# Kernel optimization log

Hardware: AMD Instinct MI355X
Metric: run time of the kernel (lower is better)

## Reference

```python
import jax, jax.numpy as jnp
import numpy as np
from jax.scipy.special import logsumexp

SPARSITY = 0.0


def setup_inputs() -> dict:
    key = jax.random.key(0)
    k1, k2, k3, k4, k5 = jax.random.split(key, 5)
    N, M = 65536, 1024
    sample = jax.random.uniform(k1, (N, 2), dtype=jnp.float32)
    mu = jax.random.uniform(k2, (M, 2), dtype=jnp.float32)
    sigma_log = jax.random.uniform(k3, (M, 2), dtype=jnp.float32)
    theta = jax.random.normal(k4, (M,), dtype=jnp.float32)
    w = jax.random.normal(k5, (M, 1), dtype=jnp.float32)
    return {"sample": sample, "mu": mu, "sigma_log": sigma_log, "theta": theta, "w": w}


def reference(sample, mu, sigma_log, theta, w):
    # Anisotropic covariance entries: gamma_j = R(theta)^T diag(sig2) R(theta)
    sig2 = jnp.exp(-2.0 * sigma_log)            # [M,2], inverse variances
    a, b = sig2[:, 0], sig2[:, 1]
    c, s = jnp.cos(theta), jnp.sin(theta)
    g11 = a * c**2 + b * s**2                   # [M]
    g12 = (a - b) * c * s                       # [M]
    g22 = a * s**2 + b * c**2                   # [M]

    # Log weights: log_softmax(w) - sum(sigma_log) (normalization factor)
    wlog = jax.nn.log_softmax(w, axis=0)[:, 0] - sigma_log.sum(axis=1)  # [M]

    # All-pairs anisotropic quadratic form, fused per-coordinate (no [N,M,2] tensor)
    dx = sample[:, None, 0] - mu[None, :, 0]    # [N,M]
    dy = sample[:, None, 1] - mu[None, :, 1]    # [N,M]
    qf = g11 * dx * dx + 2.0 * g12 * dx * dy + g22 * dy * dy  # [N,M]

    # Log-density at each sample: logsumexp over mixture components
    ll = logsumexp(wlog[None, :] - qf, axis=1)  # [N]

    # Negative log-likelihood + sparsity penalty
    nll = -ll.sum() + SPARSITY * jnp.sqrt(jax.nn.softmax(w, axis=0)).sum()
    return nll
```

## Files before the change

kernel.cpp:

```cpp
#include <hip/hip_runtime.h>
#include <math.h>

#define LOG2E 1.4426950408889634f
#define LN2   0.6931471805599453f

typedef short bf8 __attribute__((ext_vector_type(8)));
typedef float f4  __attribute__((ext_vector_type(4)));

__device__ __forceinline__ unsigned short bf_hi(float x) {
    unsigned u = __float_as_uint(x);
    return (unsigned short)((u + 0x7FFFu + ((u >> 16) & 1u)) >> 16);
}

__global__ __launch_bounds__(1024) void gm_prep(
    const float* __restrict__ mu,
    const float* __restrict__ sigma_log,
    const float* __restrict__ theta,
    const float* __restrict__ w,
    unsigned* __restrict__ grec,
    float* __restrict__ out)
{
    const int j = threadIdx.x;
    const int lane = j & 63;
    const int wid  = j >> 6;

    const float wj = w[j];
    float e = __expf(wj);
    #pragma unroll
    for (int off = 32; off > 0; off >>= 1)
        e += __shfl_down(e, off, 64);
    __shared__ float ws[16];
    if (lane == 0) ws[wid] = e;
    __syncthreads();
    float tot = 0.0f;
    #pragma unroll
    for (int k = 0; k < 16; ++k) tot += ws[k];
    const float lse = __logf(tot);

    const float sl0 = sigma_log[2 * j + 0];
    const float sl1 = sigma_log[2 * j + 1];
    const float a = __expf(-2.0f * sl0);
    const float b = __expf(-2.0f * sl1);
    const float th = theta[j];
    const float c = __cosf(th);
    const float s = __sinf(th);

    const float g11 = a * c * c + b * s * s;
    const float g12 = (a - b) * c * s;
    const float g22 = a * s * s + b * c * c;
    const float mx = mu[2 * j + 0];
    const float my = mu[2 * j + 1];
    const float wlog = wj - lse - (sl0 + sl1);

    float cf[6];
    cf[0] = -g11 * LOG2E;
    cf[1] = -2.0f * g12 * LOG2E;
    cf[2] = -g22 * LOG2E;
    cf[3] = 2.0f * (g11 * mx + g12 * my) * LOG2E;
    cf[4] = 2.0f * (g12 * mx + g22 * my) * LOG2E;
    const float F = g11 * mx * mx + 2.0f * g12 * mx * my + g22 * my * my;
    cf[5] = (wlog - F) * LOG2E;

    unsigned short r[32];
    #pragma unroll
    for (int q = 0; q < 6; ++q) {
        const unsigned short h = bf_hi(cf[q]);
        const float hf = __uint_as_float((unsigned)h << 16);
        const unsigned short l = bf_hi(cf[q] - hf);
        r[q] = h; r[6 + q] = l; r[12 + q] = h;
    }
    #pragma unroll
    for (int q = 18; q < 32; ++q) r[q] = 0;
    unsigned* dst = grec + j * 20;
    #pragma unroll
    for (int k = 0; k < 16; ++k)
        dst[k] = ((unsigned)r[2 * k + 1] << 16) | r[2 * k];

    if (j == 0) out[0] = 0.0f;
}

__global__ __launch_bounds__(1024) void gm_main(
    const float* __restrict__ sample,
    const float4* __restrict__ grec4,
    float* __restrict__ out)
{
    __shared__ __align__(16) unsigned short wrec[1024 * 40];
    __shared__ __align__(16) unsigned short srec[256 * 40];
    __shared__ float psum[16 * 256];
    __shared__ float bsum[4];

    const int tid  = threadIdx.x;
    const int lane = tid & 63;
    const int wid  = tid >> 6;
    const int quad = lane >> 4;
    const int col  = lane & 15;

    float4* wl = (float4*)wrec;
    #pragma unroll
    for (int i = 0; i < 5; ++i)
        wl[i * 1024 + tid] = grec4[i * 1024 + tid];

    if (tid < 256) {
        const float2 sv = ((const float2*)sample)[blockIdx.x * 256 + tid];
        float f[6];
        f[0] = sv.x * sv.x; f[1] = sv.x * sv.y; f[2] = sv.y * sv.y;
        f[3] = sv.x; f[4] = sv.y; f[5] = 1.0f;
        unsigned short r[32];
        #pragma unroll
        for (int q = 0; q < 6; ++q) {
            const unsigned short h = bf_hi(f[q]);
            const float hf = __uint_as_float((unsigned)h << 16);
            const unsigned short l = bf_hi(f[q] - hf);
            r[q] = h; r[6 + q] = h; r[12 + q] = l;
        }
        #pragma unroll
        for (int q = 18; q < 32; ++q) r[q] = 0;
        unsigned* dst = (unsigned*)&srec[tid * 40];
        #pragma unroll
        for (int k = 0; k < 16; ++k)
            dst[k] = ((unsigned)r[2 * k + 1] << 16) | r[2 * k];
    }
    __syncthreads();

    bf8 afrag[4];
    #pragma unroll
    for (int ct = 0; ct < 4; ++ct)
        afrag[ct] = *(const bf8*)&wrec[(wid * 64 + ct * 16 + col) * 40 + quad * 8];

    const f4 zero = {0.0f, 0.0f, 0.0f, 0.0f};
    for (int st = 0; st < 16; ++st) {
        const bf8 bfrag = *(const bf8*)&srec[(st * 16 + col) * 40 + quad * 8];
        float acc = 0.0f;
        #pragma unroll
        for (int ct = 0; ct < 4; ++ct) {
            const f4 d = __builtin_amdgcn_mfma_f32_16x16x32_bf16(
                afrag[ct], bfrag, zero, 0, 0, 0);
            acc += (__builtin_amdgcn_exp2f(d[0]) + __builtin_amdgcn_exp2f(d[1]))
                 + (__builtin_amdgcn_exp2f(d[2]) + __builtin_amdgcn_exp2f(d[3]));
        }
        acc += __shfl_xor(acc, 16, 64);
        acc += __shfl_xor(acc, 32, 64);
        if (quad == 0) psum[wid * 256 + st * 16 + col] = acc;
    }
    __syncthreads();

    if (tid < 256) {
        float t = 0.0f;
        #pragma unroll
        for (int k = 0; k < 16; ++k) t += psum[k * 256 + tid];
        float v = -LN2 * __builtin_amdgcn_logf(t);
        #pragma unroll
        for (int off = 32; off > 0; off >>= 1)
            v += __shfl_down(v, off, 64);
        if ((tid & 63) == 0) bsum[tid >> 6] = v;
    }
    __syncthreads();
    if (tid == 0)
        atomicAdd(out, (bsum[0] + bsum[1]) + (bsum[2] + bsum[3]));
}

extern "C" void kernel_launch(void* const* d_in, const int* in_sizes, int n_in,
                              void* d_out, int out_size, void* d_ws, size_t ws_size,
                              hipStream_t stream) {
    const float* sample    = (const float*)d_in[0];
    const float* mu        = (const float*)d_in[1];
    const float* sigma_log = (const float*)d_in[2];
    const float* theta     = (const float*)d_in[3];
    const float* w         = (const float*)d_in[4];
    float* out = (float*)d_out;
    unsigned* grec = (unsigned*)d_ws;

    const int N = in_sizes[0] / 2;

    gm_prep<<<1, 1024, 0, stream>>>(mu, sigma_log, theta, w, grec, out);

    const int grid = N / 256;
    gm_main<<<grid, 1024, 0, stream>>>(sample, (const float4*)grec, out);
}
```

Baseline: 77.36 us.

## Fuse prep into main kernel and reduce via cooperative grid sync

Each block now recomputes the per-component coefficient records directly into shared memory instead of loading them from a separate single-block prep kernel. This removes one kernel launch and the serial dependency on it. The global atomic accumulation is replaced by per-block partials, a cooperative grid sync, and a final reduction in block 0. The cost is redundant transcendental work in all 256 blocks and a grid-wide barrier, and the grid must fit co-resident for the cooperative launch to succeed.

Result: slower. 160.4 us (+107.4%).

```diff
diff --git a/kernel.cpp b/kernel.cpp
--- a/kernel.cpp
+++ b/kernel.cpp
@@ -1,4 +1,5 @@
 #include <hip/hip_runtime.h>
+#include <hip/hip_cooperative_groups.h>
 #include <math.h>
 
 #define LOG2E 1.4426950408889634f
@@ -12,80 +13,18 @@
     return (unsigned short)((u + 0x7FFFu + ((u >> 16) & 1u)) >> 16);
 }
 
-__global__ __launch_bounds__(1024) void gm_prep(
+__global__ __launch_bounds__(1024) void gm_coop(
+    const float* __restrict__ sample,
     const float* __restrict__ mu,
     const float* __restrict__ sigma_log,
     const float* __restrict__ theta,
     const float* __restrict__ w,
-    unsigned* __restrict__ grec,
-    float* __restrict__ out)
-{
-    const int j = threadIdx.x;
-    const int lane = j & 63;
-    const int wid  = j >> 6;
-
-    const float wj = w[j];
-    float e = __expf(wj);
-    #pragma unroll
-    for (int off = 32; off > 0; off >>= 1)
-        e += __shfl_down(e, off, 64);
-    __shared__ float ws[16];
-    if (lane == 0) ws[wid] = e;
-    __syncthreads();
-    float tot = 0.0f;
-    #pragma unroll
-    for (int k = 0; k < 16; ++k) tot += ws[k];
-    const float lse = __logf(tot);
-
-    const float sl0 = sigma_log[2 * j + 0];
-    const float sl1 = sigma_log[2 * j + 1];
-    const float a = __expf(-2.0f * sl0);
-    const float b = __expf(-2.0f * sl1);
-    const float th = theta[j];
-    const float c = __cosf(th);
-    const float s = __sinf(th);
-
-    const float g11 = a * c * c + b * s * s;
-    const float g12 = (a - b) * c * s;
-    const float g22 = a * s * s + b * c * c;
-    const float mx = mu[2 * j + 0];
-    const float my = mu[2 * j + 1];
-    const float wlog = wj - lse - (sl0 + sl1);
-
-    float cf[6];
-    cf[0] = -g11 * LOG2E;
-    cf[1] = -2.0f * g12 * LOG2E;
-    cf[2] = -g22 * LOG2E;
-    cf[3] = 2.0f * (g11 * mx + g12 * my) * LOG2E;
-    cf[4] = 2.0f * (g12 * mx + g22 * my) * LOG2E;
-    const float F = g11 * mx * mx + 2.0f * g12 * mx * my + g22 * my * my;
-    cf[5] = (wlog - F) * LOG2E;
-
-    unsigned short r[32];
-    #pragma unroll
-    for (int q = 0; q < 6; ++q) {
-        const unsigned short h = bf_hi(cf[q]);
-        const float hf = __uint_as_float((unsigned)h << 16);
-        const unsigned short l = bf_hi(cf[q] - hf);
-        r[q] = h; r[6 + q] = l; r[12 + q] = h;
-    }
-    #pragma unroll
-    for (int q = 18; q < 32; ++q) r[q] = 0;
-    unsigned* dst = grec + j * 20;
-    #pragma unroll
-    for (int k = 0; k < 16; ++k)
-        dst[k] = ((unsigned)r[2 * k + 1] << 16) | r[2 * k];
-
-    if (j == 0) out[0] = 0.0f;
-}
-
-__global__ __launch_bounds__(1024) void gm_main(
-    const float* __restrict__ sample,
-    const float4* __restrict__ grec4,
+    float* __restrict__ part,
     float* __restrict__ out)
 {
     __shared__ __align__(16) unsigned short wrec[1024 * 40];
     __shared__ __align__(16) unsigned short srec[256 * 40];
+    __shared__ float ws[16];
     __shared__ float psum[16 * 256];
     __shared__ float bsum[4];
 
@@ -95,10 +34,58 @@
     const int quad = lane >> 4;
     const int col  = lane & 15;
 
-    float4* wl = (float4*)wrec;
+    const float wj = w[tid];
+    float e = __expf(wj);
     #pragma unroll
-    for (int i = 0; i < 5; ++i)
-        wl[i * 1024 + tid] = grec4[i * 1024 + tid];
+    for (int off = 32; off > 0; off >>= 1)
+        e += __shfl_down(e, off, 64);
+    if (lane == 0) ws[wid] = e;
+    __syncthreads();
+    float tot = 0.0f;
+    #pragma unroll
+    for (int k = 0; k < 16; ++k) tot += ws[k];
+    const float lse = __logf(tot);
+
+    {
+        const float sl0 = sigma_log[2 * tid + 0];
+        const float sl1 = sigma_log[2 * tid + 1];
+        const float a = __expf(-2.0f * sl0);
+        const float b = __expf(-2.0f * sl1);
+        const float th = theta[tid];
+        const float c = __cosf(th);
+        const float s = __sinf(th);
+
+        const float g11 = a * c * c + b * s * s;
+        const float g12 = (a - b) * c * s;
+        const float g22 = a * s * s + b * c * c;
+        const float mx = mu[2 * tid + 0];
+        const float my = mu[2 * tid + 1];
+        const float wlog = wj - lse - (sl0 + sl1);
+
+        float cf[6];
+        cf[0] = -g11 * LOG2E;
+        cf[1] = -2.0f * g12 * LOG2E;
+        cf[2] = -g22 * LOG2E;
+        cf[3] = 2.0f * (g11 * mx + g12 * my) * LOG2E;
+        cf[4] = 2.0f * (g12 * mx + g22 * my) * LOG2E;
+        const float F = g11 * mx * mx + 2.0f * g12 * mx * my + g22 * my * my;
+        cf[5] = (wlog - F) * LOG2E;
+
+        unsigned short r[32];
+        #pragma unroll
+        for (int q = 0; q < 6; ++q) {
+            const unsigned short h = bf_hi(cf[q]);
+            const float hf = __uint_as_float((unsigned)h << 16);
+            const unsigned short l = bf_hi(cf[q] - hf);
+            r[q] = h; r[6 + q] = l; r[12 + q] = h;
+        }
+        #pragma unroll
+        for (int q = 18; q < 32; ++q) r[q] = 0;
+        unsigned* dst = (unsigned*)&wrec[tid * 40];
+        #pragma unroll
+        for (int k = 0; k < 16; ++k)
+            dst[k] = ((unsigned)r[2 * k + 1] << 16) | r[2 * k];
+    }
 
     if (tid < 256) {
         const float2 sv = ((const float2*)sample)[blockIdx.x * 256 + tid];
@@ -156,7 +143,22 @@
     }
     __syncthreads();
     if (tid == 0)
-        atomicAdd(out, (bsum[0] + bsum[1]) + (bsum[2] + bsum[3]));
+        part[blockIdx.x] = (bsum[0] + bsum[1]) + (bsum[2] + bsum[3]);
+
+    __threadfence();
+    cooperative_groups::this_grid().sync();
+
+    if (blockIdx.x == 0 && tid < 256) {
+        float v = part[tid];
+        #pragma unroll
+        for (int off = 32; off > 0; off >>= 1)
+            v += __shfl_down(v, off, 64);
+        __shared__ float fs[4];
+        if ((tid & 63) == 0) fs[tid >> 6] = v;
+        __syncthreads();
+        if (tid == 0)
+            out[0] = (fs[0] + fs[1]) + (fs[2] + fs[3]);
+    }
 }
 
 extern "C" void kernel_launch(void* const* d_in, const int* in_sizes, int n_in,
@@ -167,13 +169,14 @@
     const float* sigma_log = (const float*)d_in[2];
     const float* theta     = (const float*)d_in[3];
     const float* w         = (const float*)d_in[4];
-    float* out = (float*)d_out;
-    unsigned* grec = (unsigned*)d_ws;
+    float* out  = (float*)d_out;
+    float* part = (float*)d_ws;
 
     const int N = in_sizes[0] / 2;
 
-    gm_prep<<<1, 1024, 0, stream>>>(mu, sigma_log, theta, w, grec, out);
-
-    const int grid = N / 256;
-    gm_main<<<grid, 1024, 0, stream>>>(sample, (const float4*)grec, out);
+    void* args[] = {(void*)&sample, (void*)&mu, (void*)&sigma_log,
+                    (void*)&theta, (void*)&w, (void*)&part, (void*)&out};
+    hipLaunchCooperativeKernel((const void*)gm_coop,
+                               dim3(N / 256), dim3(1024),
+                               args, 0, stream);
 }
```
